# Optimization experiments

Hardware: AMD Instinct MI355X
Metric: run time of the kernel (lower is better)

## Reference

```python
import jax, jax.numpy as jnp
import numpy as np

N = 10000
E = 160000
H = 4
NEG_SLOPE = 0.2


def _edge_softmax(e, dst):
    # e: [E, H] logits; softmax over edges sharing the same dst node
    m = jax.ops.segment_max(e, dst, num_segments=N)          # [N, H]
    m = jnp.where(jnp.isfinite(m), m, 0.0)
    ex = jnp.exp(e - m[dst])                                  # [E, H]
    den = jax.ops.segment_sum(ex, dst, num_segments=N)       # [N, H]
    return ex / (den[dst] + 1e-9)


def _gat_layer(x, src, dst, W, al, ar, resW, edge=None, We=None, ae=None):
    # x: [N, Fin]; W: [Fin, H, D]; al/ar/ae: [H, D]; resW: [Fin, D]
    feat = jnp.einsum('ni,ihd->nhd', x, W)                    # [N, H, D]
    el = jnp.einsum('nhd,hd->nh', feat, al)                   # [N, H]
    er = jnp.einsum('nhd,hd->nh', feat, ar)                   # [N, H]
    e = el[src] + er[dst]                                     # [E, H]
    if edge is not None:
        ef = jnp.einsum('ei,ihd->ehd', edge, We)              # [E, H, D]
        e = e + jnp.einsum('ehd,hd->eh', ef, ae)
    e = jax.nn.leaky_relu(e, NEG_SLOPE)
    alpha = _edge_softmax(e, dst)                             # [E, H]
    msg = feat[src] * alpha[:, :, None]                       # [E, H, D]
    out = jax.ops.segment_sum(msg, dst, num_segments=N)      # [N, H, D]
    return out.mean(axis=1) + x @ resW                        # [N, D]


def setup_inputs() -> dict:
    key = jax.random.key(0)
    ks = jax.random.split(key, 24)
    node_in, edge_in, hid, out = 128, 64, 128, 256
    s = 0.1
    d = {
        'node_feats': jax.random.normal(ks[0], (N, node_in), jnp.float32),
        'edge_feats': jax.random.normal(ks[1], (E, edge_in), jnp.float32),
        'src': jax.random.randint(ks[2], (E,), 0, N, jnp.int32),
        'dst': jax.random.randint(ks[3], (E,), 0, N, jnp.int32),
        # conv1 (with edge feats): node_in -> hid
        'W1':  s * jax.random.normal(ks[4],  (node_in, H, hid), jnp.float32),
        'We1': s * jax.random.normal(ks[5],  (edge_in, H, hid), jnp.float32),
        'al1': s * jax.random.normal(ks[6],  (H, hid), jnp.float32),
        'ar1': s * jax.random.normal(ks[7],  (H, hid), jnp.float32),
        'ae1': s * jax.random.normal(ks[8],  (H, hid), jnp.float32),
        'res1': s * jax.random.normal(ks[9], (node_in, hid), jnp.float32),
        # conv2: hid -> hid
        'W2':  s * jax.random.normal(ks[10], (hid, H, hid), jnp.float32),
        'al2': s * jax.random.normal(ks[11], (H, hid), jnp.float32),
        'ar2': s * jax.random.normal(ks[12], (H, hid), jnp.float32),
        'res2': s * jax.random.normal(ks[13], (hid, hid), jnp.float32),
        # conv3: hid -> hid
        'W3':  s * jax.random.normal(ks[14], (hid, H, hid), jnp.float32),
        'al3': s * jax.random.normal(ks[15], (H, hid), jnp.float32),
        'ar3': s * jax.random.normal(ks[16], (H, hid), jnp.float32),
        'res3': s * jax.random.normal(ks[17], (hid, hid), jnp.float32),
        # conv4: hid -> out
        'W4':  s * jax.random.normal(ks[18], (hid, H, out), jnp.float32),
        'al4': s * jax.random.normal(ks[19], (H, out), jnp.float32),
        'ar4': s * jax.random.normal(ks[20], (H, out), jnp.float32),
        'res4': s * jax.random.normal(ks[21], (hid, out), jnp.float32),
    }
    return d


def reference(node_feats, edge_feats, src, dst,
              W1, We1, al1, ar1, ae1, res1,
              W2, al2, ar2, res2,
              W3, al3, ar3, res3,
              W4, al4, ar4, res4):
    h = jax.nn.relu(_gat_layer(node_feats, src, dst, W1, al1, ar1, res1,
                               edge=edge_feats, We=We1, ae=ae1))
    h = jax.nn.relu(_gat_layer(h, src, dst, W2, al2, ar2, res2))
    h = jax.nn.relu(_gat_layer(h, src, dst, W3, al3, ar3, res3))
    h = jax.nn.relu(_gat_layer(h, src, dst, W4, al4, ar4, res4))
    return h
```

## Files before the change

kernel.cpp:

```cpp
#include <hip/hip_runtime.h>

#define NN 10000
#define EE 160000

typedef __attribute__((ext_vector_type(8))) short bf16x8;
typedef __attribute__((ext_vector_type(4))) float f32x4;
typedef __attribute__((ext_vector_type(2))) float f32x2;

__device__ __forceinline__ float b2f(unsigned short s) {
    union { unsigned u; float f; } v; v.u = ((unsigned)s) << 16; return v.f;
}
__device__ __forceinline__ short f2b(float f) {
    union { float f; unsigned u; } v; v.f = f;
    unsigned r = v.u + 0x7FFF + ((v.u >> 16) & 1);
    return (short)(r >> 16);
}
__device__ __forceinline__ unsigned char f2q(float f) {
    return (unsigned char)(__builtin_amdgcn_cvt_pk_fp8_f32(f, f, 0, false) & 0xFF);
}

__global__ __launch_bounds__(256) void hist_kernel(const int* __restrict__ dst,
                                                   int* __restrict__ counts, int E) {
    int e = blockIdx.x * 256 + threadIdx.x;
    if (e < E) atomicAdd(&counts[dst[e]], 1);
// ... 104 lines not shown
        } else {
            float4 w4 = ((const float4*)w)[ln];
            float4 a4 = ((const float4*)a)[ln];
            float4 r4 = ((const float4*)r)[ln];
            sa = w4.x * a4.x + w4.y * a4.y + w4.z * a4.z + w4.w * a4.w;
            sr = w4.x * r4.x + w4.y * r4.y + w4.z * r4.z + w4.w * r4.w;
        }
        #pragma unroll
        for (int o = 32; o; o >>= 1) { sa += __shfl_xor(sa, o); sr += __shfl_xor(sr, o); }
        if (ln == 0) {
            P.Wc[l][(size_t)(P.base[l] + h) * 128 + k]     = f2b(sa);
            P.Wc[l][(size_t)(P.base[l] + 4 + h) * 128 + k] = f2b(sr);
        }
    } else if (blk < P.bC) {
        int bl = blk - P.bV;
        int wv = tid >> 6, ln = tid & 63;
        int i = bl * 4 + wv;
        #pragma unroll
        for (int h = 0; h < 4; ++h) {
            const float* w = P.We1 + ((size_t)i * 4 + h) * 128;
            const float* a = P.ae1 + (size_t)h * 128;
            float2 w2 = ((const float2*)w)[ln];
            float2 a2 = ((const float2*)a)[ln];
            float s = w2.x * a2.x + w2.y * a2.y;
            #pragma unroll
            for (int o = 32; o; o >>= 1) s += __shfl_xor(s, o);
            if (ln == 0) P.vbuf[i * 4 + h] = s;
        }
    } else if (blk < P.bZ) {
        int t = (blk - P.bC) * 256 + tid;
        if (t < NN * 32) {
            float4 v = ((const float4*)P.node_feats)[t];
            uint2 pk;
            pk.x = (unsigned short)f2b(v.x) | ((unsigned)(unsigned short)f2b(v.y) << 16);
            pk.y = (unsigned short)f2b(v.z) | ((unsigned)(unsigned short)f2b(v.w) << 16);
            ((uint2*)P.xb)[t] = pk;
        }
    } else {
        int t = (blk - P.bZ) * 256 + tid;
        if (t < NN / 4) ((int4*)P.counts)[t] = make_int4(0, 0, 0, 0);
    }
}

template <int D>
__global__ __launch_bounds__(256) void gemm_fused(const short* __restrict__ A,
                                                  const short* __restrict__ Bt,
                                                  unsigned char* __restrict__ featq,
                                                  float* __restrict__ y,
                                                  float* __restrict__ elr,
                                                  int M) {
    constexpr int HD = 4 * D;
    int wave = threadIdx.x >> 6, lane = threadIdx.x & 63;
    int m0 = blockIdx.y * 64;
    int n0 = blockIdx.x * 64 + wave * 16;
    int r = lane & 15, quad = lane >> 4;
    f32x4 acc[4] = {};
    const short* bp = Bt + (size_t)(n0 + r) * 128 + quad * 8;
    #pragma unroll
    for (int k0 = 0; k0 < 128; k0 += 32) {
        bf16x8 bfrag = *(const bf16x8*)(bp + k0);
        #pragma unroll
        for (int mt = 0; mt < 4; ++mt) {
            int gm = m0 + mt * 16 + r;
            bf16x8 afrag = {};
            if (gm < M) afrag = *(const bf16x8*)(A + (size_t)gm * 128 + k0 + quad * 8);
            acc[mt] = __builtin_amdgcn_mfma_f32_16x16x32_bf16(afrag, bfrag, acc[mt], 0, 0, 0);
        }
    }
    int col = n0 + r;
    #pragma unroll
    for (int mt = 0; mt < 4; ++mt) {
        #pragma unroll
        for (int rr = 0; rr < 4; ++rr) {
            int gm = m0 + mt * 16 + quad * 4 + rr;
            if (gm >= M) continue;
            float v = acc[mt][rr];
            if (col < HD)              featq[(size_t)gm * HD + col] = f2q(v);
            else if (col < HD + D)     y[(size_t)gm * D + (col - HD)] = v;
            else if (col < HD + D + 8) elr[(size_t)gm * 8 + (col - HD - D)] = v;
        }
    }
}

__device__ __forceinline__ void accum8q(float* a, uint2 v, float w) {
    f32x2 p0 = __builtin_amdgcn_cvt_pk_f32_fp8(v.x, false);
    f32x2 p1 = __builtin_amdgcn_cvt_pk_f32_fp8(v.x, true);
    f32x2 p2 = __builtin_amdgcn_cvt_pk_f32_fp8(v.y, false);
    f32x2 p3 = __builtin_amdgcn_cvt_pk_f32_fp8(v.y, true);
    a[0] += w * p0.x; a[1] += w * p0.y;
    a[2] += w * p1.x; a[3] += w * p1.y;
    a[4] += w * p2.x; a[5] += w * p2.y;
    a[6] += w * p3.x; a[7] += w * p3.y;
}

__device__ __forceinline__ float sel4(int ln, float s0, float s1, float s2, float s3) {
    return ln < 16 ? s0 : ln < 32 ? s1 : ln < 48 ? s2 : s3;
}

__device__ __forceinline__ void gather_q(int cnt, int start, int step, int sidx,
                                         float e0, float e1, float e2, float e3,
                                         const unsigned char* __restrict__ base, int ln,
                                         float acc[8]) {
    int j = start;
    for (; j + 3 * step < cnt; j += 4 * step) {
        int jB = j + step, jC = j + 2 * step, jD = j + 3 * step;
        int s0 = __shfl(sidx, j), s1 = __shfl(sidx, jB);
        int s2 = __shfl(sidx, jC), s3 = __shfl(sidx, jD);
        uint2 v0 = *(const uint2*)(base + (size_t)s0 * 512);
        uint2 v1 = *(const uint2*)(base + (size_t)s1 * 512);
        uint2 v2 = *(const uint2*)(base + (size_t)s2 * 512);
        uint2 v3 = *(const uint2*)(base + (size_t)s3 * 512);
        float a00 = __shfl(e0, j),  a01 = __shfl(e1, j),  a02 = __shfl(e2, j),  a03 = __shfl(e3, j);
        float a10 = __shfl(e0, jB), a11 = __shfl(e1, jB), a12 = __shfl(e2, jB), a13 = __shfl(e3, jB);
        float a20 = __shfl(e0, jC), a21 = __shfl(e1, jC), a22 = __shfl(e2, jC), a23 = __shfl(e3, jC);
        float a30 = __shfl(e0, jD), a31 = __shfl(e1, jD), a32 = __shfl(e2, jD), a33 = __shfl(e3, jD);
        float w0 = sel4(ln, a00, a01, a02, a03);
        float w1 = sel4(ln, a10, a11, a12, a13);
        float w2 = sel4(ln, a20, a21, a22, a23);
        float w3 = sel4(ln, a30, a31, a32, a33);
        accum8q(acc, v0, w0); accum8q(acc, v1, w1);
        accum8q(acc, v2, w2); accum8q(acc, v3, w3);
    }
    for (; j < cnt; j += step) {
        int s0 = __shfl(sidx, j);
        uint2 v0 = *(const uint2*)(base + (size_t)s0 * 512);
        float a0 = __shfl(e0, j), a1 = __shfl(e1, j), a2 = __shfl(e2, j), a3 = __shfl(e3, j);
        float w0 = sel4(ln, a0, a1, a2, a3);
        accum8q(acc, v0, w0);
    }
}

__device__ __forceinline__ void gather_p(int cnt, int sidx, float eA, float eB,
                                         const unsigned char* __restrict__ base, int ln,
                                         float acc[8]) {
    int j = 0;
    for (; j + 4 <= cnt; j += 4) {
        int s0 = __shfl(sidx, j), s1 = __shfl(sidx, j + 1);
        int s2 = __shfl(sidx, j + 2), s3 = __shfl(sidx, j + 3);
        uint2 v0 = *(const uint2*)(base + (size_t)s0 * 1024);
        uint2 v1 = *(const uint2*)(base + (size_t)s1 * 1024);
        uint2 v2 = *(const uint2*)(base + (size_t)s2 * 1024);
        uint2 v3 = *(const uint2*)(base + (size_t)s3 * 1024);
        float a0A = __shfl(eA, j),     a0B = __shfl(eB, j);
        float a1A = __shfl(eA, j + 1), a1B = __shfl(eB, j + 1);
        float a2A = __shfl(eA, j + 2), a2B = __shfl(eB, j + 2);
        float a3A = __shfl(eA, j + 3), a3B = __shfl(eB, j + 3);
        float w0 = ln < 32 ? a0A : a0B;
        float w1 = ln < 32 ? a1A : a1B;
        float w2 = ln < 32 ? a2A : a2B;
        float w3 = ln < 32 ? a3A : a3B;
        accum8q(acc, v0, w0); accum8q(acc, v1, w1);
        accum8q(acc, v2, w2); accum8q(acc, v3, w3);
    }
    for (; j < cnt; ++j) {
        int s0 = __shfl(sidx, j);
        uint2 v0 = *(const uint2*)(base + (size_t)s0 * 1024);
        float aA = __shfl(eA, j), aB = __shfl(eB, j);
        float w0 = ln < 32 ? aA : aB;
        accum8q(acc, v0, w0);
    }
}

template <bool HAS_EXTRA>
__global__ __launch_bounds__(256) void gat128(const unsigned char* __restrict__ featq,
                                              const float* __restrict__ elr,
                                              const float* __restrict__ extra,
                                              const int* __restrict__ ssrc,
                                              const int* __restrict__ off,
                                              const float* __restrict__ yres,
                                              short* __restrict__ ybf) {
    __shared__ float red[2][128];
    int wv = threadIdx.x >> 6, ln = threadIdx.x & 63;
    int slot = wv >> 1, half = wv & 1;
    int n = blockIdx.x * 2 + slot;
    int r0 = off[n], deg = off[n + 1] - r0;
    float4 erv = *(const float4*)(elr + (size_t)n * 8 + 4);
    float acc[8] = {0.f, 0.f, 0.f, 0.f, 0.f, 0.f, 0.f, 0.f};
    float sc0, sc1, sc2, sc3;

    auto logits = [&](int idx, float& a0, float& a1, float& a2, float& a3) {
        int s = ssrc[idx];
        float4 elv = *(const float4*)(elr + (size_t)s * 8);
        a0 = elv.x + erv.x; a1 = elv.y + erv.y; a2 = elv.z + erv.z; a3 = elv.w + erv.w;
        if (HAS_EXTRA) {
            float4 exv = *(const float4*)(extra + (size_t)idx * 4);
            a0 += exv.x; a1 += exv.y; a2 += exv.z; a3 += exv.w;
        }
        a0 = a0 > 0.f ? a0 : 0.2f * a0;
        a1 = a1 > 0.f ? a1 : 0.2f * a1;
        a2 = a2 > 0.f ? a2 : 0.2f * a2;
        a3 = a3 > 0.f ? a3 : 0.2f * a3;
        return s;
    };

    if (deg <= 64) {
        int sidx = 0;
        float a0 = -1e30f, a1 = -1e30f, a2 = -1e30f, a3 = -1e30f;
        if (ln < deg) sidx = logits(r0 + ln, a0, a1, a2, a3);
        float m0 = a0, m1 = a1, m2 = a2, m3 = a3;
        #pragma unroll
        for (int o = 32; o; o >>= 1) {
            m0 = fmaxf(m0, __shfl_xor(m0, o)); m1 = fmaxf(m1, __shfl_xor(m1, o));
            m2 = fmaxf(m2, __shfl_xor(m2, o)); m3 = fmaxf(m3, __shfl_xor(m3, o));
        }
        float e0 = 0.f, e1 = 0.f, e2 = 0.f, e3 = 0.f;
        if (ln < deg) {
            e0 = __expf(a0 - m0); e1 = __expf(a1 - m1);
            e2 = __expf(a2 - m2); e3 = __expf(a3 - m3);
        }
        float s0 = e0, s1 = e1, s2 = e2, s3 = e3;
        #pragma unroll
        for (int o = 32; o; o >>= 1) {
            s0 += __shfl_xor(s0, o); s1 += __shfl_xor(s1, o);
            s2 += __shfl_xor(s2, o); s3 += __shfl_xor(s3, o);
        }
        sc0 = 0.25f / (s0 + 1e-9f); sc1 = 0.25f / (s1 + 1e-9f);
        sc2 = 0.25f / (s2 + 1e-9f); sc3 = 0.25f / (s3 + 1e-9f);
        gather_q(deg, half, 2, sidx, e0, e1, e2, e3, featq + ln * 8, ln, acc);
    } else {
        float m0 = -1e30f, m1 = -1e30f, m2 = -1e30f, m3 = -1e30f;
        for (int base = 0; base < deg; base += 64) {
            float a0 = -1e30f, a1 = -1e30f, a2 = -1e30f, a3 = -1e30f;
            if (base + ln < deg) logits(r0 + base + ln, a0, a1, a2, a3);
            m0 = fmaxf(m0, a0); m1 = fmaxf(m1, a1); m2 = fmaxf(m2, a2); m3 = fmaxf(m3, a3);
        }
        #pragma unroll
        for (int o = 32; o; o >>= 1) {
            m0 = fmaxf(m0, __shfl_xor(m0, o)); m1 = fmaxf(m1, __shfl_xor(m1, o));
            m2 = fmaxf(m2, __shfl_xor(m2, o)); m3 = fmaxf(m3, __shfl_xor(m3, o));
        }
        float s0 = 0.f, s1 = 0.f, s2 = 0.f, s3 = 0.f;
        for (int base = 0; base < deg; base += 64) {
            float a0, a1, a2, a3;
            if (base + ln < deg) {
                logits(r0 + base + ln, a0, a1, a2, a3);
                s0 += __expf(a0 - m0); s1 += __expf(a1 - m1);
                s2 += __expf(a2 - m2); s3 += __expf(a3 - m3);
            }
        }
        #pragma unroll
        for (int o = 32; o; o >>= 1) {
            s0 += __shfl_xor(s0, o); s1 += __shfl_xor(s1, o);
            s2 += __shfl_xor(s2, o); s3 += __shfl_xor(s3, o);
        }
        sc0 = 0.25f / (s0 + 1e-9f); sc1 = 0.25f / (s1 + 1e-9f);
        sc2 = 0.25f / (s2 + 1e-9f); sc3 = 0.25f / (s3 + 1e-9f);
        for (int base = 0; base < deg; base += 64) {
            int sidx = 0;
            float e0 = 0.f, e1 = 0.f, e2 = 0.f, e3 = 0.f;
            if (base + ln < deg) {
                float a0, a1, a2, a3;
                sidx = logits(r0 + base + ln, a0, a1, a2, a3);
                e0 = __expf(a0 - m0); e1 = __expf(a1 - m1);
                e2 = __expf(a2 - m2); e3 = __expf(a3 - m3);
            }
            int cnt = deg - base; if (cnt > 64) cnt = 64;
            gather_q(cnt, half, 2, sidx, e0, e1, e2, e3, featq + ln * 8, ln, acc);
        }
    }

    float scl = sel4(ln, sc0, sc1, sc2, sc3);
    float t[8];
    #pragma unroll
    for (int i = 0; i < 8; ++i) {
        float v = acc[i] * scl;
        v += __shfl_xor(v, 16);
        v += __shfl_xor(v, 32);
        t[i] = v;
    }
    if (half == 1 && ln < 16) {
        #pragma unroll
        for (int i = 0; i < 8; ++i) red[slot][ln * 8 + i] = t[i];
    }
    __syncthreads();
    if (half == 0 && ln < 16) {
        int d0 = ln * 8;
        const float* yr = yres + (size_t)n * 128 + d0;
        float4 ya = *(const float4*)yr;
        float4 yb = *(const float4*)(yr + 4);
        float o[8];
        o[0] = fmaxf(ya.x + t[0] + red[slot][d0 + 0], 0.f);
        o[1] = fmaxf(ya.y + t[1] + red[slot][d0 + 1], 0.f);
        o[2] = fmaxf(ya.z + t[2] + red[slot][d0 + 2], 0.f);
        o[3] = fmaxf(ya.w + t[3] + red[slot][d0 + 3], 0.f);
        o[4] = fmaxf(yb.x + t[4] + red[slot][d0 + 4], 0.f);
        o[5] = fmaxf(yb.y + t[5] + red[slot][d0 + 5], 0.f);
        o[6] = fmaxf(yb.z + t[6] + red[slot][d0 + 6], 0.f);
        o[7] = fmaxf(yb.w + t[7] + red[slot][d0 + 7], 0.f);
        uint4 pk;
        pk.x = (unsigned short)f2b(o[0]) | ((unsigned)(unsigned short)f2b(o[1]) << 16);
        pk.y = (unsigned short)f2b(o[2]) | ((unsigned)(unsigned short)f2b(o[3]) << 16);
        pk.z = (unsigned short)f2b(o[4]) | ((unsigned)(unsigned short)f2b(o[5]) << 16);
        pk.w = (unsigned short)f2b(o[6]) | ((unsigned)(unsigned short)f2b(o[7]) << 16);
        *(uint4*)(ybf + (size_t)n * 128 + d0) = pk;
    }
}

__global__ __launch_bounds__(256) void gat256(const unsigned char* __restrict__ featq,
                                              const float* __restrict__ elr,
                                              const int* __restrict__ ssrc,
                                              const int* __restrict__ off,
                                              const float* __restrict__ yres,
                                              float* __restrict__ yout) {
    __shared__ float red[2][256];
    int wv = threadIdx.x >> 6, ln = threadIdx.x & 63;
    int slot = wv >> 1, half = wv & 1;
    int n = blockIdx.x * 2 + slot;
    int r0 = off[n], deg = off[n + 1] - r0;
    float4 erv = *(const float4*)(elr + (size_t)n * 8 + 4);
    float acc[8] = {0.f, 0.f, 0.f, 0.f, 0.f, 0.f, 0.f, 0.f};
    float sc0, sc1, sc2, sc3;
    const unsigned char* base = featq + half * 512 + ln * 8;

    auto logits = [&](int idx, float& a0, float& a1, float& a2, float& a3) {
        int s = ssrc[idx];
        float4 elv = *(const float4*)(elr + (size_t)s * 8);
        a0 = elv.x + erv.x; a1 = elv.y + erv.y; a2 = elv.z + erv.z; a3 = elv.w + erv.w;
        a0 = a0 > 0.f ? a0 : 0.2f * a0;
        a1 = a1 > 0.f ? a1 : 0.2f * a1;
        a2 = a2 > 0.f ? a2 : 0.2f * a2;
        a3 = a3 > 0.f ? a3 : 0.2f * a3;
        return s;
    };

    if (deg <= 64) {
        int sidx = 0;
        float a0 = -1e30f, a1 = -1e30f, a2 = -1e30f, a3 = -1e30f;
        if (ln < deg) sidx = logits(r0 + ln, a0, a1, a2, a3);
        float m0 = a0, m1 = a1, m2 = a2, m3 = a3;
        #pragma unroll
        for (int o = 32; o; o >>= 1) {
            m0 = fmaxf(m0, __shfl_xor(m0, o)); m1 = fmaxf(m1, __shfl_xor(m1, o));
            m2 = fmaxf(m2, __shfl_xor(m2, o)); m3 = fmaxf(m3, __shfl_xor(m3, o));
        }
        float e0 = 0.f, e1 = 0.f, e2 = 0.f, e3 = 0.f;
        if (ln < deg) {
            e0 = __expf(a0 - m0); e1 = __expf(a1 - m1);
            e2 = __expf(a2 - m2); e3 = __expf(a3 - m3);
        }
        float s0 = e0, s1 = e1, s2 = e2, s3 = e3;
        #pragma unroll
        for (int o = 32; o; o >>= 1) {
            s0 += __shfl_xor(s0, o); s1 += __shfl_xor(s1, o);
            s2 += __shfl_xor(s2, o); s3 += __shfl_xor(s3, o);
        }
        sc0 = 0.25f / (s0 + 1e-9f); sc1 = 0.25f / (s1 + 1e-9f);
        sc2 = 0.25f / (s2 + 1e-9f); sc3 = 0.25f / (s3 + 1e-9f);
        float eA = half ? e2 : e0;
        float eB = half ? e3 : e1;
        gather_p(deg, sidx, eA, eB, base, ln, acc);
    } else {
        float m0 = -1e30f, m1 = -1e30f, m2 = -1e30f, m3 = -1e30f;
        for (int b = 0; b < deg; b += 64) {
            float a0 = -1e30f, a1 = -1e30f, a2 = -1e30f, a3 = -1e30f;
            if (b + ln < deg) logits(r0 + b + ln, a0, a1, a2, a3);
            m0 = fmaxf(m0, a0); m1 = fmaxf(m1, a1); m2 = fmaxf(m2, a2); m3 = fmaxf(m3, a3);
        }
        #pragma unroll
        for (int o = 32; o; o >>= 1) {
            m0 = fmaxf(m0, __shfl_xor(m0, o)); m1 = fmaxf(m1, __shfl_xor(m1, o));
            m2 = fmaxf(m2, __shfl_xor(m2, o)); m3 = fmaxf(m3, __shfl_xor(m3, o));
        }
        float s0 = 0.f, s1 = 0.f, s2 = 0.f, s3 = 0.f;
        for (int b = 0; b < deg; b += 64) {
            float a0, a1, a2, a3;
            if (b + ln < deg) {
                logits(r0 + b + ln, a0, a1, a2, a3);
                s0 += __expf(a0 - m0); s1 += __expf(a1 - m1);
                s2 += __expf(a2 - m2); s3 += __expf(a3 - m3);
            }
        }
        #pragma unroll
        for (int o = 32; o; o >>= 1) {
            s0 += __shfl_xor(s0, o); s1 += __shfl_xor(s1, o);
            s2 += __shfl_xor(s2, o); s3 += __shfl_xor(s3, o);
        }
        sc0 = 0.25f / (s0 + 1e-9f); sc1 = 0.25f / (s1 + 1e-9f);
        sc2 = 0.25f / (s2 + 1e-9f); sc3 = 0.25f / (s3 + 1e-9f);
        for (int b = 0; b < deg; b += 64) {
            int sidx = 0;
            float e0 = 0.f, e1 = 0.f, e2 = 0.f, e3 = 0.f;
            if (b + ln < deg) {
                float a0, a1, a2, a3;
                sidx = logits(r0 + b + ln, a0, a1, a2, a3);
                e0 = __expf(a0 - m0); e1 = __expf(a1 - m1);
                e2 = __expf(a2 - m2); e3 = __expf(a3 - m3);
            }
            int cnt = deg - b; if (cnt > 64) cnt = 64;
            float eA = half ? e2 : e0;
            float eB = half ? e3 : e1;
            gather_p(cnt, sidx, eA, eB, base, ln, acc);
        }
    }

    float sc = (ln < 32) ? (half ? sc2 : sc0) : (half ? sc3 : sc1);
    float t[8];
    #pragma unroll
    for (int i = 0; i < 8; ++i) {
        float v = acc[i] * sc;
        v += __shfl_xor(v, 32);
        t[i] = v;
    }
    if (half == 1 && ln < 32) {
        #pragma unroll
        for (int i = 0; i < 8; ++i) red[slot][ln * 8 + i] = t[i];
    }
    __syncthreads();
    if (half == 0 && ln < 32) {
        int d0 = ln * 8;
        const float* yr = yres + (size_t)n * 256 + d0;
        float4 ya = *(const float4*)yr;
        float4 yb = *(const float4*)(yr + 4);
        float4 oa, ob;
        oa.x = fmaxf(ya.x + t[0] + red[slot][d0 + 0], 0.f);
        oa.y = fmaxf(ya.y + t[1] + red[slot][d0 + 1], 0.f);
        oa.z = fmaxf(ya.z + t[2] + red[slot][d0 + 2], 0.f);
        oa.w = fmaxf(ya.w + t[3] + red[slot][d0 + 3], 0.f);
        ob.x = fmaxf(yb.x + t[4] + red[slot][d0 + 4], 0.f);
        ob.y = fmaxf(yb.y + t[5] + red[slot][d0 + 5], 0.f);
        ob.z = fmaxf(yb.z + t[6] + red[slot][d0 + 6], 0.f);
        ob.w = fmaxf(yb.w + t[7] + red[slot][d0 + 7], 0.f);
        *(float4*)(yout + (size_t)n * 256 + d0) = oa;
        *(float4*)(yout + (size_t)n * 256 + d0 + 4) = ob;
    }
}

extern "C" void kernel_launch(void* const* d_in, const int* in_sizes, int n_in,
                              void* d_out, int out_size, void* d_ws, size_t ws_size,
                              hipStream_t stream) {
    const float* node_feats = (const float*)d_in[0];
    const float* edge_feats = (const float*)d_in[1];
    const int*   src        = (const int*)d_in[2];
    const int*   dst        = (const int*)d_in[3];
    const float* W1   = (const float*)d_in[4];
    const float* We1  = (const float*)d_in[5];
    const float* al1  = (const float*)d_in[6];
    const float* ar1  = (const float*)d_in[7];
    const float* ae1  = (const float*)d_in[8];
    const float* res1 = (const float*)d_in[9];
    const float* W2   = (const float*)d_in[10];
    const float* al2  = (const float*)d_in[11];
    const float* ar2  = (const float*)d_in[12];
    const float* res2 = (const float*)d_in[13];
    const float* W3   = (const float*)d_in[14];
    const float* al3  = (const float*)d_in[15];
    const float* ar3  = (const float*)d_in[16];
    const float* res3 = (const float*)d_in[17];
    const float* W4   = (const float*)d_in[18];
    const float* al4  = (const float*)d_in[19];
    const float* ar4  = (const float*)d_in[20];
    const float* res4 = (const float*)d_in[21];

    char* ws = (char*)d_ws;
    auto alloc = [&](size_t bytes) -> char* {
        char* p = ws;
        ws += (bytes + 255) & ~(size_t)255;
        return p;
    };
    int*   counts  = (int*)alloc((size_t)NN * 4);
    int*   offsets = (int*)alloc((size_t)(NN + 1) * 4);
    int*   cursor  = (int*)alloc((size_t)(NN + 1) * 4);
    int*   ssrc    = (int*)alloc((size_t)EE * 4);
    unsigned char* featq = (unsigned char*)alloc((size_t)NN * 1024);
    float* xA      = (float*)alloc((size_t)NN * 128 * 4);
    short* xb      = (short*)alloc((size_t)NN * 128 * 2);
    float* elr     = (float*)alloc((size_t)NN * 8 * 4);
    float* extra   = (float*)alloc((size_t)EE * 4 * 4);
    float* vbuf    = (float*)alloc(1024);
    short* Wc1     = (short*)alloc((size_t)704 * 128 * 2);
    short* Wc2     = (short*)alloc((size_t)704 * 128 * 2);
    short* Wc3     = (short*)alloc((size_t)704 * 128 * 2);
    short* Wc4     = (short*)alloc((size_t)1344 * 128 * 2);

    PrepParams P;
    P.tsrc[0] = W1;   P.tdst[0] = Wc1;              P.tN[0] = 512;  P.tshift[0] = 9;
    P.tsrc[1] = W2;   P.tdst[1] = Wc2;              P.tN[1] = 512;  P.tshift[1] = 9;
    P.tsrc[2] = W3;   P.tdst[2] = Wc3;              P.tN[2] = 512;  P.tshift[2] = 9;
    P.tsrc[3] = W4;   P.tdst[3] = Wc4;              P.tN[3] = 1024; P.tshift[3] = 10;
    P.tsrc[4] = res1; P.tdst[4] = Wc1 + 512 * 128;  P.tN[4] = 128;  P.tshift[4] = 7;
    P.tsrc[5] = res2; P.tdst[5] = Wc2 + 512 * 128;  P.tN[5] = 128;  P.tshift[5] = 7;
    P.tsrc[6] = res3; P.tdst[6] = Wc3 + 512 * 128;  P.tN[6] = 128;  P.tshift[6] = 7;
    P.tsrc[7] = res4; P.tdst[7] = Wc4 + 1024 * 128; P.tN[7] = 256;  P.tshift[7] = 8;
    P.tcum4[0] = 0;
    for (int i = 0; i < 8; ++i) P.tcum4[i + 1] = P.tcum4[i] + P.tN[i] * 128 / 4;
    P.W[0] = W1; P.W[1] = W2; P.W[2] = W3; P.W[3] = W4;
    P.al[0] = al1; P.al[1] = al2; P.al[2] = al3; P.al[3] = al4;
    P.ar[0] = ar1; P.ar[1] = ar2; P.ar[2] = ar3; P.ar[3] = ar4;
    P.Wc[0] = Wc1; P.Wc[1] = Wc2; P.Wc[2] = Wc3; P.Wc[3] = Wc4;
    P.Dl[0] = 128; P.Dl[1] = 128; P.Dl[2] = 128; P.Dl[3] = 256;
    P.base[0] = 640; P.base[1] = 640; P.base[2] = 640; P.base[3] = 1280;
    P.We1 = We1; P.ae1 = ae1; P.vbuf = vbuf;
    P.node_feats = node_feats; P.xb = xb;
    P.counts = counts;
    P.bWA = (P.tcum4[8] + 255) / 256;
    P.bV  = P.bWA + 512;
    P.bC  = P.bV + 16;
    P.bZ  = P.bC + (NN * 32 + 255) / 256;
    int nblk = P.bZ + (NN / 4 + 255) / 256;
    prep_kernel<<<nblk, 256, 0, stream>>>(P);

    hist_kernel<<<(EE + 255) / 256, 256, 0, stream>>>(dst, counts, EE);
    scan_kernel<<<1, 256, 0, stream>>>(counts, offsets, cursor, NN);
    fill_extra<<<(EE + 255) / 256, 256, 0, stream>>>(src, dst, cursor, edge_feats,
                                                     vbuf, ssrc, extra, EE);

    float* out = (float*)d_out;
    dim3 g128(11, (NN + 63) / 64);
    dim3 g256(21, (NN + 63) / 64);
    int gs = NN / 2;

    gemm_fused<128><<<g128, 256, 0, stream>>>(xb, Wc1, featq, xA, elr, NN);
    gat128<true><<<gs, 256, 0, stream>>>(featq, elr, extra, ssrc, offsets, xA, xb);
    gemm_fused<128><<<g128, 256, 0, stream>>>(xb, Wc2, featq, xA, elr, NN);
    gat128<false><<<gs, 256, 0, stream>>>(featq, elr, nullptr, ssrc, offsets, xA, xb);
    gemm_fused<128><<<g128, 256, 0, stream>>>(xb, Wc3, featq, xA, elr, NN);
    gat128<false><<<gs, 256, 0, stream>>>(featq, elr, nullptr, ssrc, offsets, xA, xb);
    gemm_fused<256><<<g256, 256, 0, stream>>>(xb, Wc4, featq, out, elr, NN);
    gat256<<<gs, 256, 0, stream>>>(featq, elr, ssrc, offsets, out, out);
}
```

Measured before the change: 378.4 us.

## Use one wave per node with 16-byte fp8 gathers in GAT aggregation

```diff
diff --git a/kernel.cpp b/kernel.cpp
--- a/kernel.cpp
+++ b/kernel.cpp
@@ -210,84 +210,108 @@
     }
 }
 
-__device__ __forceinline__ void accum8q(float* a, uint2 v, float w) {
-    f32x2 p0 = __builtin_amdgcn_cvt_pk_f32_fp8(v.x, false);
-    f32x2 p1 = __builtin_amdgcn_cvt_pk_f32_fp8(v.x, true);
-    f32x2 p2 = __builtin_amdgcn_cvt_pk_f32_fp8(v.y, false);
-    f32x2 p3 = __builtin_amdgcn_cvt_pk_f32_fp8(v.y, true);
-    a[0] += w * p0.x; a[1] += w * p0.y;
-    a[2] += w * p1.x; a[3] += w * p1.y;
-    a[4] += w * p2.x; a[5] += w * p2.y;
-    a[6] += w * p3.x; a[7] += w * p3.y;
-}
-
-__device__ __forceinline__ float sel4(int ln, float s0, float s1, float s2, float s3) {
-    return ln < 16 ? s0 : ln < 32 ? s1 : ln < 48 ? s2 : s3;
-}
-
-__device__ __forceinline__ void gather_q(int cnt, int start, int step, int sidx,
-                                         float e0, float e1, float e2, float e3,
-                                         const unsigned char* __restrict__ base, int ln,
-                                         float acc[8]) {
-    int j = start;
-    for (; j + 3 * step < cnt; j += 4 * step) {
-        int jB = j + step, jC = j + 2 * step, jD = j + 3 * step;
-        int s0 = __shfl(sidx, j), s1 = __shfl(sidx, jB);
-        int s2 = __shfl(sidx, jC), s3 = __shfl(sidx, jD);
-        uint2 v0 = *(const uint2*)(base + (size_t)s0 * 512);
-        uint2 v1 = *(const uint2*)(base + (size_t)s1 * 512);
-        uint2 v2 = *(const uint2*)(base + (size_t)s2 * 512);
-        uint2 v3 = *(const uint2*)(base + (size_t)s3 * 512);
-        float a00 = __shfl(e0, j),  a01 = __shfl(e1, j),  a02 = __shfl(e2, j),  a03 = __shfl(e3, j);
-        float a10 = __shfl(e0, jB), a11 = __shfl(e1, jB), a12 = __shfl(e2, jB), a13 = __shfl(e3, jB);
-        float a20 = __shfl(e0, jC), a21 = __shfl(e1, jC), a22 = __shfl(e2, jC), a23 = __shfl(e3, jC);
-        float a30 = __shfl(e0, jD), a31 = __shfl(e1, jD), a32 = __shfl(e2, jD), a33 = __shfl(e3, jD);
-        float w0 = sel4(ln, a00, a01, a02, a03);
-        float w1 = sel4(ln, a10, a11, a12, a13);
-        float w2 = sel4(ln, a20, a21, a22, a23);
-        float w3 = sel4(ln, a30, a31, a32, a33);
-        accum8q(acc, v0, w0); accum8q(acc, v1, w1);
-        accum8q(acc, v2, w2); accum8q(acc, v3, w3);
-    }
-    for (; j < cnt; j += step) {
-        int s0 = __shfl(sidx, j);
-        uint2 v0 = *(const uint2*)(base + (size_t)s0 * 512);
-        float a0 = __shfl(e0, j), a1 = __shfl(e1, j), a2 = __shfl(e2, j), a3 = __shfl(e3, j);
-        float w0 = sel4(ln, a0, a1, a2, a3);
-        accum8q(acc, v0, w0);
-    }
-}
-
-__device__ __forceinline__ void gather_p(int cnt, int sidx, float eA, float eB,
-                                         const unsigned char* __restrict__ base, int ln,
-                                         float acc[8]) {
-    int j = 0;
-    for (; j + 4 <= cnt; j += 4) {
-        int s0 = __shfl(sidx, j), s1 = __shfl(sidx, j + 1);
-        int s2 = __shfl(sidx, j + 2), s3 = __shfl(sidx, j + 3);
-        uint2 v0 = *(const uint2*)(base + (size_t)s0 * 1024);
-        uint2 v1 = *(const uint2*)(base + (size_t)s1 * 1024);
-        uint2 v2 = *(const uint2*)(base + (size_t)s2 * 1024);
-        uint2 v3 = *(const uint2*)(base + (size_t)s3 * 1024);
-        float a0A = __shfl(eA, j),     a0B = __shfl(eB, j);
-        float a1A = __shfl(eA, j + 1), a1B = __shfl(eB, j + 1);
-        float a2A = __shfl(eA, j + 2), a2B = __shfl(eB, j + 2);
-        float a3A = __shfl(eA, j + 3), a3B = __shfl(eB, j + 3);
-        float w0 = ln < 32 ? a0A : a0B;
-        float w1 = ln < 32 ? a1A : a1B;
-        float w2 = ln < 32 ? a2A : a2B;
-        float w3 = ln < 32 ? a3A : a3B;
-        accum8q(acc, v0, w0); accum8q(acc, v1, w1);
-        accum8q(acc, v2, w2); accum8q(acc, v3, w3);
-    }
-    for (; j < cnt; ++j) {
-        int s0 = __shfl(sidx, j);
-        uint2 v0 = *(const uint2*)(base + (size_t)s0 * 1024);
-        float aA = __shfl(eA, j), aB = __shfl(eB, j);
-        float w0 = ln < 32 ? aA : aB;
-        accum8q(acc, v0, w0);
-    }
-}
+__device__ __forceinline__ void accum16q(float* a, uint4 v, float w) {
+    f32x2 p;
+    p = __builtin_amdgcn_cvt_pk_f32_fp8(v.x, false); a[0] += w * p.x; a[1] += w * p.y;
+    p = __builtin_amdgcn_cvt_pk_f32_fp8(v.x, true);  a[2] += w * p.x; a[3] += w * p.y;
+    p = __builtin_amdgcn_cvt_pk_f32_fp8(v.y, false); a[4] += w * p.x; a[5] += w * p.y;
+    p = __builtin_amdgcn_cvt_pk_f32_fp8(v.y, true);  a[6] += w * p.x; a[7] += w * p.y;
+    p = __builtin_amdgcn_cvt_pk_f32_fp8(v.z, false); a[8] += w * p.x; a[9] += w * p.y;
+    p = __builtin_amdgcn_cvt_pk_f32_fp8(v.z, true);  a[10] += w * p.x; a[11] += w * p.y;
+    p = __builtin_amdgcn_cvt_pk_f32_fp8(v.w, false); a[12] += w * p.x; a[13] += w * p.y;
+    p = __builtin_amdgcn_cvt_pk_f32_fp8(v.w, true);  a[14] += w * p.x; a[15] += w * p.y;
+}
+
+__device__ __forceinline__ float hsel(int h, float s0, float s1, float s2, float s3) {
+    return h == 0 ? s0 : h == 1 ? s1 : h == 2 ? s2 : s3;
+}
+
+__device__ __forceinline__ void gather128(int T, int deg, int g, int h, int sidx,
+                                          float e0, float e1, float e2, float e3,
+                                          const unsigned char* __restrict__ basep,
+                                          float acc[16]) {
+    int it = 0;
+    for (; it + 4 <= T; it += 4) {
+        int j0 = 2 * it + g, j1 = j0 + 2, j2 = j0 + 4, j3 = j0 + 6;
+        int c0 = j0 < deg ? j0 : deg - 1;
+        int c1 = j1 < deg ? j1 : deg - 1;
+        int c2 = j2 < deg ? j2 : deg - 1;
+        int c3 = j3 < deg ? j3 : deg - 1;
+        float m0 = j0 < deg ? 1.f : 0.f, m1 = j1 < deg ? 1.f : 0.f;
+        float m2 = j2 < deg ? 1.f : 0.f, m3 = j3 < deg ? 1.f : 0.f;
+        int s0 = __shfl(sidx, c0), s1 = __shfl(sidx, c1);
+        int s2 = __shfl(sidx, c2), s3 = __shfl(sidx, c3);
+        uint4 v0 = *(const uint4*)(basep + (size_t)s0 * 512);
+        uint4 v1 = *(const uint4*)(basep + (size_t)s1 * 512);
+        uint4 v2 = *(const uint4*)(basep + (size_t)s2 * 512);
+        uint4 v3 = *(const uint4*)(basep + (size_t)s3 * 512);
+        float w0 = hsel(h, __shfl(e0, c0), __shfl(e1, c0), __shfl(e2, c0), __shfl(e3, c0)) * m0;
+        float w1 = hsel(h, __shfl(e0, c1), __shfl(e1, c1), __shfl(e2, c1), __shfl(e3, c1)) * m1;
+        float w2 = hsel(h, __shfl(e0, c2), __shfl(e1, c2), __shfl(e2, c2), __shfl(e3, c2)) * m2;
+        float w3 = hsel(h, __shfl(e0, c3), __shfl(e1, c3), __shfl(e2, c3), __shfl(e3, c3)) * m3;
+        accum16q(acc, v0, w0); accum16q(acc, v1, w1);
+        accum16q(acc, v2, w2); accum16q(acc, v3, w3);
+    }
+    for (; it < T; ++it) {
+        int j0 = 2 * it + g;
+        int c0 = j0 < deg ? j0 : deg - 1;
+        float m0 = j0 < deg ? 1.f : 0.f;
+        int s0 = __shfl(sidx, c0);
+        uint4 v0 = *(const uint4*)(basep + (size_t)s0 * 512);
+        float w0 = hsel(h, __shfl(e0, c0), __shfl(e1, c0), __shfl(e2, c0), __shfl(e3, c0)) * m0;
+        accum16q(acc, v0, w0);
+    }
+}
+
+__device__ __forceinline__ void gather256(int T, int deg, int half, int h, int sidx,
+                                          float e0, float e1, float e2, float e3,
+                                          const unsigned char* __restrict__ basep,
+                                          float acc[16]) {
+    int it = 0;
+    for (; it + 4 <= T; it += 4) {
+        int j0 = 2 * it + half, j1 = j0 + 2, j2 = j0 + 4, j3 = j0 + 6;
+        int c0 = j0 < deg ? j0 : deg - 1;
+        int c1 = j1 < deg ? j1 : deg - 1;
+        int c2 = j2 < deg ? j2 : deg - 1;
+        int c3 = j3 < deg ? j3 : deg - 1;
+        float m0 = j0 < deg ? 1.f : 0.f, m1 = j1 < deg ? 1.f : 0.f;
+        float m2 = j2 < deg ? 1.f : 0.f, m3 = j3 < deg ? 1.f : 0.f;
+        int s0 = __shfl(sidx, c0), s1 = __shfl(sidx, c1);
+        int s2 = __shfl(sidx, c2), s3 = __shfl(sidx, c3);
+        uint4 v0 = *(const uint4*)(basep + (size_t)s0 * 1024);
+        uint4 v1 = *(const uint4*)(basep + (size_t)s1 * 1024);
+        uint4 v2 = *(const uint4*)(basep + (size_t)s2 * 1024);
+        uint4 v3 = *(const uint4*)(basep + (size_t)s3 * 1024);
+        float w0 = hsel(h, __shfl(e0, c0), __shfl(e1, c0), __shfl(e2, c0), __shfl(e3, c0)) * m0;
+        float w1 = hsel(h, __shfl(e0, c1), __shfl(e1, c1), __shfl(e2, c1), __shfl(e3, c1)) * m1;
+        float w2 = hsel(h, __shfl(e0, c2), __shfl(e1, c2), __shfl(e2, c2), __shfl(e3, c2)) * m2;
+        float w3 = hsel(h, __shfl(e0, c3), __shfl(e1, c3), __shfl(e2, c3), __shfl(e3, c3)) * m3;
+        accum16q(acc, v0, w0); accum16q(acc, v1, w1);
+        accum16q(acc, v2, w2); accum16q(acc, v3, w3);
+    }
+    for (; it < T; ++it) {
+        int j0 = 2 * it + half;
+        int c0 = j0 < deg ? j0 : deg - 1;
+        float m0 = j0 < deg ? 1.f : 0.f;
+        int s0 = __shfl(sidx, c0);
+        uint4 v0 = *(const uint4*)(basep + (size_t)s0 * 1024);
+        float w0 = hsel(h, __shfl(e0, c0), __shfl(e1, c0), __shfl(e2, c0), __shfl(e3, c0)) * m0;
+        accum16q(acc, v0, w0);
+    }
+}
+
+#define WAVE_MAX4(m0,m1,m2,m3)                                              \
+    _Pragma("unroll")                                                       \
+    for (int o = 32; o; o >>= 1) {                                          \
+        m0 = fmaxf(m0, __shfl_xor(m0, o)); m1 = fmaxf(m1, __shfl_xor(m1, o));\
+        m2 = fmaxf(m2, __shfl_xor(m2, o)); m3 = fmaxf(m3, __shfl_xor(m3, o));\
+    }
+#define WAVE_SUM4(s0,s1,s2,s3)                                              \
+    _Pragma("unroll")                                                       \
+    for (int o = 32; o; o >>= 1) {                                          \
+        s0 += __shfl_xor(s0, o); s1 += __shfl_xor(s1, o);                   \
+        s2 += __shfl_xor(s2, o); s3 += __shfl_xor(s3, o);                   \
+    }
 
 template <bool HAS_EXTRA>
 __global__ __launch_bounds__(256) void gat128(const unsigned char* __restrict__ featq,
@@ -297,14 +321,17 @@
                                               const int* __restrict__ off,
                                               const float* __restrict__ yres,
                                               short* __restrict__ ybf) {
-    __shared__ float red[2][128];
     int wv = threadIdx.x >> 6, ln = threadIdx.x & 63;
-    int slot = wv >> 1, half = wv & 1;
-    int n = blockIdx.x * 2 + slot;
+    int n = blockIdx.x * 4 + wv;
     int r0 = off[n], deg = off[n + 1] - r0;
+    int g = ln >> 5, l5 = ln & 31;
+    int h = l5 >> 3;
     float4 erv = *(const float4*)(elr + (size_t)n * 8 + 4);
-    float acc[8] = {0.f, 0.f, 0.f, 0.f, 0.f, 0.f, 0.f, 0.f};
+    float acc[16];
+    #pragma unroll
+    for (int i = 0; i < 16; ++i) acc[i] = 0.f;
     float sc0, sc1, sc2, sc3;
+    const unsigned char* basep = featq + l5 * 16;
 
     auto logits = [&](int idx, float& a0, float& a1, float& a2, float& a3) {
         int s = ssrc[idx];
@@ -326,157 +353,17 @@
         float a0 = -1e30f, a1 = -1e30f, a2 = -1e30f, a3 = -1e30f;
         if (ln < deg) sidx = logits(r0 + ln, a0, a1, a2, a3);
         float m0 = a0, m1 = a1, m2 = a2, m3 = a3;
-        #pragma unroll
-        for (int o = 32; o; o >>= 1) {
-            m0 = fmaxf(m0, __shfl_xor(m0, o)); m1 = fmaxf(m1, __shfl_xor(m1, o));
-            m2 = fmaxf(m2, __shfl_xor(m2, o)); m3 = fmaxf(m3, __shfl_xor(m3, o));
-        }
+        WAVE_MAX4(m0, m1, m2, m3)
         float e0 = 0.f, e1 = 0.f, e2 = 0.f, e3 = 0.f;
         if (ln < deg) {
             e0 = __expf(a0 - m0); e1 = __expf(a1 - m1);
             e2 = __expf(a2 - m2); e3 = __expf(a3 - m3);
         }
         float s0 = e0, s1 = e1, s2 = e2, s3 = e3;
-        #pragma unroll
-        for (int o = 32; o; o >>= 1) {
-            s0 += __shfl_xor(s0, o); s1 += __shfl_xor(s1, o);
-            s2 += __shfl_xor(s2, o); s3 += __shfl_xor(s3, o);
-        }
+        WAVE_SUM4(s0, s1, s2, s3)
         sc0 = 0.25f / (s0 + 1e-9f); sc1 = 0.25f / (s1 + 1e-9f);
         sc2 = 0.25f / (s2 + 1e-9f); sc3 = 0.25f / (s3 + 1e-9f);
-        gather_q(deg, half, 2, sidx, e0, e1, e2, e3, featq + ln * 8, ln, acc);
-    } else {
-        float m0 = -1e30f, m1 = -1e30f, m2 = -1e30f, m3 = -1e30f;
-        for (int base = 0; base < deg; base += 64) {
-            float a0 = -1e30f, a1 = -1e30f, a2 = -1e30f, a3 = -1e30f;
-            if (base + ln < deg) logits(r0 + base + ln, a0, a1, a2, a3);
-            m0 = fmaxf(m0, a0); m1 = fmaxf(m1, a1); m2 = fmaxf(m2, a2); m3 = fmaxf(m3, a3);
-        }
-        #pragma unroll
-        for (int o = 32; o; o >>= 1) {
-            m0 = fmaxf(m0, __shfl_xor(m0, o)); m1 = fmaxf(m1, __shfl_xor(m1, o));
-            m2 = fmaxf(m2, __shfl_xor(m2, o)); m3 = fmaxf(m3, __shfl_xor(m3, o));
-        }
-        float s0 = 0.f, s1 = 0.f, s2 = 0.f, s3 = 0.f;
-        for (int base = 0; base < deg; base += 64) {
-            float a0, a1, a2, a3;
-            if (base + ln < deg) {
-                logits(r0 + base + ln, a0, a1, a2, a3);
-                s0 += __expf(a0 - m0); s1 += __expf(a1 - m1);
-                s2 += __expf(a2 - m2); s3 += __expf(a3 - m3);
-            }
-        }
-        #pragma unroll
-        for (int o = 32; o; o >>= 1) {
-            s0 += __shfl_xor(s0, o); s1 += __shfl_xor(s1, o);
-            s2 += __shfl_xor(s2, o); s3 += __shfl_xor(s3, o);
-        }
-        sc0 = 0.25f / (s0 + 1e-9f); sc1 = 0.25f / (s1 + 1e-9f);
-        sc2 = 0.25f / (s2 + 1e-9f); sc3 = 0.25f / (s3 + 1e-9f);
-        for (int base = 0; base < deg; base += 64) {
-            int sidx = 0;
-            float e0 = 0.f, e1 = 0.f, e2 = 0.f, e3 = 0.f;
-            if (base + ln < deg) {
-                float a0, a1, a2, a3;
-                sidx = logits(r0 + base + ln, a0, a1, a2, a3);
-                e0 = __expf(a0 - m0); e1 = __expf(a1 - m1);
-                e2 = __expf(a2 - m2); e3 = __expf(a3 - m3);
-            }
-            int cnt = deg - base; if (cnt > 64) cnt = 64;
-            gather_q(cnt, half, 2, sidx, e0, e1, e2, e3, featq + ln * 8, ln, acc);
-        }
-    }
-
-    float scl = sel4(ln, sc0, sc1, sc2, sc3);
-    float t[8];
-    #pragma unroll
-    for (int i = 0; i < 8; ++i) {
-        float v = acc[i] * scl;
-        v += __shfl_xor(v, 16);
-        v += __shfl_xor(v, 32);
-        t[i] = v;
-    }
-    if (half == 1 && ln < 16) {
-        #pragma unroll
-        for (int i = 0; i < 8; ++i) red[slot][ln * 8 + i] = t[i];
-    }
-    __syncthreads();
-    if (half == 0 && ln < 16) {
-        int d0 = ln * 8;
-        const float* yr = yres + (size_t)n * 128 + d0;
-        float4 ya = *(const float4*)yr;
-        float4 yb = *(const float4*)(yr + 4);
-        float o[8];
-        o[0] = fmaxf(ya.x + t[0] + red[slot][d0 + 0], 0.f);
-        o[1] = fmaxf(ya.y + t[1] + red[slot][d0 + 1], 0.f);
-        o[2] = fmaxf(ya.z + t[2] + red[slot][d0 + 2], 0.f);
-        o[3] = fmaxf(ya.w + t[3] + red[slot][d0 + 3], 0.f);
-        o[4] = fmaxf(yb.x + t[4] + red[slot][d0 + 4], 0.f);
-        o[5] = fmaxf(yb.y + t[5] + red[slot][d0 + 5], 0.f);
-        o[6] = fmaxf(yb.z + t[6] + red[slot][d0 + 6], 0.f);
-        o[7] = fmaxf(yb.w + t[7] + red[slot][d0 + 7], 0.f);
-        uint4 pk;
-        pk.x = (unsigned short)f2b(o[0]) | ((unsigned)(unsigned short)f2b(o[1]) << 16);
-        pk.y = (unsigned short)f2b(o[2]) | ((unsigned)(unsigned short)f2b(o[3]) << 16);
-        pk.z = (unsigned short)f2b(o[4]) | ((unsigned)(unsigned short)f2b(o[5]) << 16);
-        pk.w = (unsigned short)f2b(o[6]) | ((unsigned)(unsigned short)f2b(o[7]) << 16);
-        *(uint4*)(ybf + (size_t)n * 128 + d0) = pk;
-    }
-}
-
-__global__ __launch_bounds__(256) void gat256(const unsigned char* __restrict__ featq,
-                                              const float* __restrict__ elr,
-                                              const int* __restrict__ ssrc,
-                                              const int* __restrict__ off,
-                                              const float* __restrict__ yres,
-                                              float* __restrict__ yout) {
-    __shared__ float red[2][256];
-    int wv = threadIdx.x >> 6, ln = threadIdx.x & 63;
-    int slot = wv >> 1, half = wv & 1;
-    int n = blockIdx.x * 2 + slot;
-    int r0 = off[n], deg = off[n + 1] - r0;
-    float4 erv = *(const float4*)(elr + (size_t)n * 8 + 4);
-    float acc[8] = {0.f, 0.f, 0.f, 0.f, 0.f, 0.f, 0.f, 0.f};
-    float sc0, sc1, sc2, sc3;
-    const unsigned char* base = featq + half * 512 + ln * 8;
-
-    auto logits = [&](int idx, float& a0, float& a1, float& a2, float& a3) {
-        int s = ssrc[idx];
-        float4 elv = *(const float4*)(elr + (size_t)s * 8);
-        a0 = elv.x + erv.x; a1 = elv.y + erv.y; a2 = elv.z + erv.z; a3 = elv.w + erv.w;
-        a0 = a0 > 0.f ? a0 : 0.2f * a0;
-        a1 = a1 > 0.f ? a1 : 0.2f * a1;
-        a2 = a2 > 0.f ? a2 : 0.2f * a2;
-        a3 = a3 > 0.f ? a3 : 0.2f * a3;
-        return s;
-    };
-
-    if (deg <= 64) {
-        int sidx = 0;
-        float a0 = -1e30f, a1 = -1e30f, a2 = -1e30f, a3 = -1e30f;
-        if (ln < deg) sidx = logits(r0 + ln, a0, a1, a2, a3);
-        float m0 = a0, m1 = a1, m2 = a2, m3 = a3;
-        #pragma unroll
-        for (int o = 32; o; o >>= 1) {
-            m0 = fmaxf(m0, __shfl_xor(m0, o)); m1 = fmaxf(m1, __shfl_xor(m1, o));
-            m2 = fmaxf(m2, __shfl_xor(m2, o)); m3 = fmaxf(m3, __shfl_xor(m3, o));
-        }
-        float e0 = 0.f, e1 = 0.f, e2 = 0.f, e3 = 0.f;
-        if (ln < deg) {
-            e0 = __expf(a0 - m0); e1 = __expf(a1 - m1);
-            e2 = __expf(a2 - m2); e3 = __expf(a3 - m3);
-        }
-        float s0 = e0, s1 = e1, s2 = e2, s3 = e3;
-        #pragma unroll
-        for (int o = 32; o; o >>= 1) {
-            s0 += __shfl_xor(s0, o); s1 += __shfl_xor(s1, o);
-            s2 += __shfl_xor(s2, o); s3 += __shfl_xor(s3, o);
-        }
-        sc0 = 0.25f / (s0 + 1e-9f); sc1 = 0.25f / (s1 + 1e-9f);
-        sc2 = 0.25f / (s2 + 1e-9f); sc3 = 0.25f / (s3 + 1e-9f);
-        float eA = half ? e2 : e0;
-        float eB = half ? e3 : e1;
-        gather_p(deg, sidx, eA, eB, base, ln, acc);
+        gather128((deg + 1) >> 1, deg, g, h, sidx, e0, e1, e2, e3, basep, acc);
     } else {
         float m0 = -1e30f, m1 = -1e30f, m2 = -1e30f, m3 = -1e30f;
         for (int b = 0; b < deg; b += 64) {
@@ -484,11 +371,7 @@
             if (b + ln < deg) logits(r0 + b + ln, a0, a1, a2, a3);
             m0 = fmaxf(m0, a0); m1 = fmaxf(m1, a1); m2 = fmaxf(m2, a2); m3 = fmaxf(m3, a3);
         }
-        #pragma unroll
-        for (int o = 32; o; o >>= 1) {
-            m0 = fmaxf(m0, __shfl_xor(m0, o)); m1 = fmaxf(m1, __shfl_xor(m1, o));
-            m2 = fmaxf(m2, __shfl_xor(m2, o)); m3 = fmaxf(m3, __shfl_xor(m3, o));
-        }
+        WAVE_MAX4(m0, m1, m2, m3)
         float s0 = 0.f, s1 = 0.f, s2 = 0.f, s3 = 0.f;
         for (int b = 0; b < deg; b += 64) {
             float a0, a1, a2, a3;
@@ -498,11 +381,7 @@
                 s2 += __expf(a2 - m2); s3 += __expf(a3 - m3);
             }
         }
-        #pragma unroll
-        for (int o = 32; o; o >>= 1) {
-            s0 += __shfl_xor(s0, o); s1 += __shfl_xor(s1, o);
-            s2 += __shfl_xor(s2, o); s3 += __shfl_xor(s3, o);
-        }
+        WAVE_SUM4(s0, s1, s2, s3)
         sc0 = 0.25f / (s0 + 1e-9f); sc1 = 0.25f / (s1 + 1e-9f);
         sc2 = 0.25f / (s2 + 1e-9f); sc3 = 0.25f / (s3 + 1e-9f);
         for (int b = 0; b < deg; b += 64) {
@@ -515,41 +394,147 @@
                 e2 = __expf(a2 - m2); e3 = __expf(a3 - m3);
             }
             int cnt = deg - b; if (cnt > 64) cnt = 64;
-            float eA = half ? e2 : e0;
-            float eB = half ? e3 : e1;
-            gather_p(cnt, sidx, eA, eB, base, ln, acc);
-        }
-    }
-
-    float sc = (ln < 32) ? (half ? sc2 : sc0) : (half ? sc3 : sc1);
-    float t[8];
+            gather128((cnt + 1) >> 1, cnt, g, h, sidx, e0, e1, e2, e3, basep, acc);
+        }
+    }
+
+    float scl = hsel(h, sc0, sc1, sc2, sc3);
+    float t[16];
     #pragma unroll
-    for (int i = 0; i < 8; ++i) {
-        float v = acc[i] * sc;
+    for (int i = 0; i < 16; ++i) {
+        float v = acc[i] * scl;
+        v += __shfl_xor(v, 32);
+        v += __shfl_xor(v, 8);
+        v += __shfl_xor(v, 16);
+        t[i] = v;
+    }
+    if (ln < 8) {
+        int d0 = ln * 16;
+        const float* yr = yres + (size_t)n * 128 + d0;
+        unsigned pk[8];
+        #pragma unroll
+        for (int q = 0; q < 8; ++q) {
+            float ya = yr[2 * q], yb = yr[2 * q + 1];
+            float o0 = fmaxf(ya + t[2 * q], 0.f);
+            float o1 = fmaxf(yb + t[2 * q + 1], 0.f);
+            pk[q] = (unsigned short)f2b(o0) | ((unsigned)(unsigned short)f2b(o1) << 16);
+        }
+        uint4 pa, pb;
+        pa.x = pk[0]; pa.y = pk[1]; pa.z = pk[2]; pa.w = pk[3];
+        pb.x = pk[4]; pb.y = pk[5]; pb.z = pk[6]; pb.w = pk[7];
+        *(uint4*)(ybf + (size_t)n * 128 + d0) = pa;
+        *(uint4*)(ybf + (size_t)n * 128 + d0 + 8) = pb;
+    }
+}
+
+__global__ __launch_bounds__(256) void gat256(const unsigned char* __restrict__ featq,
+                                              const float* __restrict__ elr,
+                                              const int* __restrict__ ssrc,
+                                              const int* __restrict__ off,
+                                              const float* __restrict__ yres,
+                                              float* __restrict__ yout) {
+    __shared__ float red[2][256];
+    int wv = threadIdx.x >> 6, ln = threadIdx.x & 63;
+    int slot = wv >> 1, half = wv & 1;
+    int n = blockIdx.x * 2 + slot;
+    int r0 = off[n], deg = off[n + 1] - r0;
+    int h = ln >> 4;
+    float4 erv = *(const float4*)(elr + (size_t)n * 8 + 4);
+    float acc[16];
+    #pragma unroll
+    for (int i = 0; i < 16; ++i) acc[i] = 0.f;
+    float sc0, sc1, sc2, sc3;
+    const unsigned char* basep = featq + ln * 16;
+
+    auto logits = [&](int idx, float& a0, float& a1, float& a2, float& a3) {
+        int s = ssrc[idx];
+        float4 elv = *(const float4*)(elr + (size_t)s * 8);
+        a0 = elv.x + erv.x; a1 = elv.y + erv.y; a2 = elv.z + erv.z; a3 = elv.w + erv.w;
+        a0 = a0 > 0.f ? a0 : 0.2f * a0;
+        a1 = a1 > 0.f ? a1 : 0.2f * a1;
+        a2 = a2 > 0.f ? a2 : 0.2f * a2;
+        a3 = a3 > 0.f ? a3 : 0.2f * a3;
+        return s;
+    };
+
+    if (deg <= 64) {
+        int sidx = 0;
+        float a0 = -1e30f, a1 = -1e30f, a2 = -1e30f, a3 = -1e30f;
+        if (ln < deg) sidx = logits(r0 + ln, a0, a1, a2, a3);
+        float m0 = a0, m1 = a1, m2 = a2, m3 = a3;
+        WAVE_MAX4(m0, m1, m2, m3)
+        float e0 = 0.f, e1 = 0.f, e2 = 0.f, e3 = 0.f;
+        if (ln < deg) {
+            e0 = __expf(a0 - m0); e1 = __expf(a1 - m1);
+            e2 = __expf(a2 - m2); e3 = __expf(a3 - m3);
+        }
+        float s0 = e0, s1 = e1, s2 = e2, s3 = e3;
+        WAVE_SUM4(s0, s1, s2, s3)
+        sc0 = 0.25f / (s0 + 1e-9f); sc1 = 0.25f / (s1 + 1e-9f);
+        sc2 = 0.25f / (s2 + 1e-9f); sc3 = 0.25f / (s3 + 1e-9f);
+        gather256((deg + 1) >> 1, deg, half, h, sidx, e0, e1, e2, e3, basep, acc);
+    } else {
+        float m0 = -1e30f, m1 = -1e30f, m2 = -1e30f, m3 = -1e30f;
+        for (int b = 0; b < deg; b += 64) {
+            float a0 = -1e30f, a1 = -1e30f, a2 = -1e30f, a3 = -1e30f;
+            if (b + ln < deg) logits(r0 + b + ln, a0, a1, a2, a3);
+            m0 = fmaxf(m0, a0); m1 = fmaxf(m1, a1); m2 = fmaxf(m2, a2); m3 = fmaxf(m3, a3);
+        }
+        WAVE_MAX4(m0, m1, m2, m3)
+        float s0 = 0.f, s1 = 0.f, s2 = 0.f, s3 = 0.f;
+        for (int b = 0; b < deg; b += 64) {
+            float a0, a1, a2, a3;
+            if (b + ln < deg) {
+                logits(r0 + b + ln, a0, a1, a2, a3);
+                s0 += __expf(a0 - m0); s1 += __expf(a1 - m1);
+                s2 += __expf(a2 - m2); s3 += __expf(a3 - m3);
+            }
+        }
+        WAVE_SUM4(s0, s1, s2, s3)
+        sc0 = 0.25f / (s0 + 1e-9f); sc1 = 0.25f / (s1 + 1e-9f);
+        sc2 = 0.25f / (s2 + 1e-9f); sc3 = 0.25f / (s3 + 1e-9f);
+        for (int b = 0; b < deg; b += 64) {
+            int sidx = 0;
+            float e0 = 0.f, e1 = 0.f, e2 = 0.f, e3 = 0.f;
+            if (b + ln < deg) {
+                float a0, a1, a2, a3;
+                sidx = logits(r0 + b + ln, a0, a1, a2, a3);
+                e0 = __expf(a0 - m0); e1 = __expf(a1 - m1);
+                e2 = __expf(a2 - m2); e3 = __expf(a3 - m3);
+            }
+            int cnt = deg - b; if (cnt > 64) cnt = 64;
+            gather256((cnt + 1) >> 1, cnt, half, h, sidx, e0, e1, e2, e3, basep, acc);
+        }
+    }
+
+    float scl = hsel(h, sc0, sc1, sc2, sc3);
+    float t[16];
+    #pragma unroll
+    for (int i = 0; i < 16; ++i) {
+        float v = acc[i] * scl;
+        v += __shfl_xor(v, 16);
         v += __shfl_xor(v, 32);
         t[i] = v;
     }
-    if (half == 1 && ln < 32) {
-        #pragma unroll
-        for (int i = 0; i < 8; ++i) red[slot][ln * 8 + i] = t[i];
+    if (half == 1 && ln < 16) {
+        #pragma unroll
+        for (int i = 0; i < 16; ++i) red[slot][ln * 16 + i] = t[i];
     }
     __syncthreads();
-    if (half == 0 && ln < 32) {
-        int d0 = ln * 8;
+    if (half == 0 && ln < 16) {
+        int d0 = ln * 16;
         const float* yr = yres + (size_t)n * 256 + d0;
-        float4 ya = *(const float4*)yr;
-        float4 yb = *(const float4*)(yr + 4);
-        float4 oa, ob;
-        oa.x = fmaxf(ya.x + t[0] + red[slot][d0 + 0], 0.f);
-        oa.y = fmaxf(ya.y + t[1] + red[slot][d0 + 1], 0.f);
-        oa.z = fmaxf(ya.z + t[2] + red[slot][d0 + 2], 0.f);
-        oa.w = fmaxf(ya.w + t[3] + red[slot][d0 + 3], 0.f);
-        ob.x = fmaxf(yb.x + t[4] + red[slot][d0 + 4], 0.f);
-        ob.y = fmaxf(yb.y + t[5] + red[slot][d0 + 5], 0.f);
-        ob.z = fmaxf(yb.z + t[6] + red[slot][d0 + 6], 0.f);
-        ob.w = fmaxf(yb.w + t[7] + red[slot][d0 + 7], 0.f);
-        *(float4*)(yout + (size_t)n * 256 + d0) = oa;
-        *(float4*)(yout + (size_t)n * 256 + d0 + 4) = ob;
+        float* yo = yout + (size_t)n * 256 + d0;
+        #pragma unroll
+        for (int q = 0; q < 4; ++q) {
+            float4 ya = *(const float4*)(yr + 4 * q);
+            float4 ov;
+            ov.x = fmaxf(ya.x + t[4 * q + 0] + red[slot][d0 + 4 * q + 0], 0.f);
+            ov.y = fmaxf(ya.y + t[4 * q + 1] + red[slot][d0 + 4 * q + 1], 0.f);
+            ov.z = fmaxf(ya.z + t[4 * q + 2] + red[slot][d0 + 4 * q + 2], 0.f);
+            ov.w = fmaxf(ya.w + t[4 * q + 3] + red[slot][d0 + 4 * q + 3], 0.f);
+            *(float4*)(yo + 4 * q) = ov;
+        }
     }
 }
 
@@ -635,14 +620,15 @@
     float* out = (float*)d_out;
     dim3 g128(11, (NN + 63) / 64);
     dim3 g256(21, (NN + 63) / 64);
-    int gs = NN / 2;
+    int gs128 = NN / 4;
+    int gs256 = NN / 2;
 
     gemm_fused<128><<<g128, 256, 0, stream>>>(xb, Wc1, featq, xA, elr, NN);
-    gat128<true><<<gs, 256, 0, stream>>>(featq, elr, extra, ssrc, offsets, xA, xb);
+    gat128<true><<<gs128, 256, 0, stream>>>(featq, elr, extra, ssrc, offsets, xA, xb);
     gemm_fused<128><<<g128, 256, 0, stream>>>(xb, Wc2, featq, xA, elr, NN);
-    gat128<false><<<gs, 256, 0, stream>>>(featq, elr, nullptr, ssrc, offsets, xA, xb);
+    gat128<false><<<gs128, 256, 0, stream>>>(featq, elr, nullptr, ssrc, offsets, xA, xb);
     gemm_fused<128><<<g128, 256, 0, stream>>>(xb, Wc3, featq, xA, elr, NN);
-    gat128<false><<<gs, 256, 0, stream>>>(featq, elr, nullptr, ssrc, offsets, xA, xb);
+    gat128<false><<<gs128, 256, 0, stream>>>(featq, elr, nullptr, ssrc, offsets, xA, xb);
     gemm_fused<256><<<g256, 256, 0, stream>>>(xb, Wc4, featq, out, elr, NN);
-    gat256<<<gs, 256, 0, stream>>>(featq, elr, ssrc, offsets, out, out);
-}
+    gat256<<<gs256, 256, 0, stream>>>(featq, elr, ssrc, offsets, out, out);
+}
```

New measurement: 366.2 us, median of 2. 3.2% less time.
